# Kernel optimization log

Measured on AMD Instinct MI355X. Metric: run time of the kernel, lower is better.

The kernel has to match this reference:

```python
import jax, jax.numpy as jnp
import numpy as np

B, S, D, H = 8, 2048, 512, 8
DH = D // H


def setup_inputs() -> dict:
    key = jax.random.key(0)
    ks = jax.random.split(key, 7)
    scale = 1.0 / np.sqrt(DH)
    return {
        "sequences": jax.random.normal(ks[0], (B, S, D), dtype=jnp.float32),
        # torch Linear weights: [H, d_head, d_head] (out, in) per head
        "Wq": jax.random.uniform(ks[1], (H, DH, DH), jnp.float32, -scale, scale),
        "bq": jax.random.uniform(ks[2], (H, DH), jnp.float32, -scale, scale),
        "Wk": jax.random.uniform(ks[3], (H, DH, DH), jnp.float32, -scale, scale),
        "bk": jax.random.uniform(ks[4], (H, DH), jnp.float32, -scale, scale),
        "Wv": jax.random.uniform(ks[5], (H, DH, DH), jnp.float32, -scale, scale),
        "bv": jax.random.uniform(ks[6], (H, DH), jnp.float32, -scale, scale),
    }


def reference(sequences, Wq, bq, Wk, bk, Wv, bv):
    # split heads: [B, S, H, DH]
    x = sequences.reshape(B, S, H, DH)
    # per-head Linear: y = x @ W^T + b  (torch convention W is [out, in])
    q = jnp.einsum('bshd,hed->bshe', x, Wq) + bq  # [B,S,H,DH]
    k = jnp.einsum('bshd,hed->bshe', x, Wk) + bk
    v = jnp.einsum('bshd,hed->bshe', x, Wv) + bv
    scores = jnp.einsum('bshe,bthe->bhst', q, k) / jnp.sqrt(jnp.float32(DH))
    attn = jax.nn.softmax(scores, axis=-1)  # [B,H,S,S]
    out = jnp.einsum('bhst,bthd->bshd', attn, v)  # [B,S,H,DH]
    return out.reshape(B, S, D)
```

## Files before the change

### kernel.cpp

```cpp
#include <hip/hip_runtime.h>
#include <hip/hip_bf16.h>
#include <math.h>

#define Bc 8
#define Sc 2048
#define Dc 512
#define Hc 8
#define DHc 64
#define KVB 64
#define NT (Sc / KVB)

#define QSCALE 0.18033688011112042f

typedef __attribute__((ext_vector_type(8))) short short8;
typedef __attribute__((ext_vector_type(4))) float f32x4;
typedef __attribute__((ext_vector_type(16))) float f32x16;
typedef unsigned short u16;
typedef unsigned int u32;

static __device__ __forceinline__ u16 f2bf(float f) {
    union { float f; u32 u; } v; v.f = f;
    u32 r = v.u + 0x7fffu + ((v.u >> 16) & 1u);
    return (u16)(r >> 16);
}

static __device__ __forceinline__ u32 cvtpk(float lo, float hi) {
    u32 r; asm("v_cvt_pk_bf16_f32 %0, %1, %2" : "=v"(r) : "v"(lo), "v"(hi)); return r;
}

static __device__ __forceinline__ void plswap(u32& a, u32& b) {
    asm("v_permlane32_swap_b32 %0, %1" : "+v"(a), "+v"(b));
}

static __device__ __forceinline__ short8 pack8v(const float4& a0, const float4& a1) {
    union { u32 w[4]; short8 s; } u;
    u.w[0] = cvtpk(a0.x, a0.y);
    u.w[1] = cvtpk(a0.z, a0.w);
    u.w[2] = cvtpk(a1.x, a1.y);
    u.w[3] = cvtpk(a1.z, a1.w);
    return u.s;
}

static __device__ __forceinline__ short8 mk8(u32 a, u32 b, u32 c, u32 d) {
    union { u32 w[4]; short8 s; } u;
    u.w[0] = a; u.w[1] = b; u.w[2] = c; u.w[3] = d;
    return u.s;
}

#define GLDS16(g, s) \
    __builtin_amdgcn_global_load_lds((const __attribute__((address_space(1))) void*)(g), \
                                     (__attribute__((address_space(3))) void*)(s), 16, 0, 0)

__global__ __launch_bounds__(256) void prep(
    const float* __restrict__ Wq, const float* __restrict__ bq,
    const float* __restrict__ Wk, const float* __restrict__ bk,
    const float* __restrict__ Wv, const float* __restrict__ bv,
    u16* __restrict__ wb, float* __restrict__ bb)
{
    const int gid = blockIdx.x * 256 + threadIdx.x;
    const float* Ws[3] = {Wq, Wk, Wv};
    const int lane = gid & 63, ds = (gid >> 6) & 1, et = (gid >> 7) & 3;
    const int h = (gid >> 9) & 7, m = gid >> 12;
    const int col = lane & 15, grp = lane >> 4;
    const float* src = Ws[m] + ((size_t)h * DHc + et * 16 + col) * DHc + ds * 32 + grp * 8;
    float4 a0 = ((const float4*)src)[0], a1 = ((const float4*)src)[1];
    const float sc = (m == 0) ? QSCALE : 1.0f;
    union { u32 w[4]; int4 v; } u;
    u.w[0] = cvtpk(a0.x * sc, a0.y * sc);
    u.w[1] = cvtpk(a0.z * sc, a0.w * sc);
    u.w[2] = cvtpk(a1.x * sc, a1.y * sc);
    u.w[3] = cvtpk(a1.z * sc, a1.w * sc);
    *(int4*)(wb + (size_t)gid * 8) = u.v;

    if (gid < 3 * Hc * DHc) {
        const float* bs[3] = {bq, bk, bv};
        const int bm = gid >> 9, rest = gid & 511;
        bb[gid] = bs[bm][rest] * (bm == 0 ? QSCALE : 1.0f);
    }
}

__global__ __launch_bounds__(256) void qkv_proj(
    const float* __restrict__ x, const u16* __restrict__ wb,
    const float* __restrict__ bb,
    u16* __restrict__ qo, u16* __restrict__ ko, u16* __restrict__ vto)
{
    const int tile = blockIdx.x;
    const int h    = blockIdx.y;
    const int tid  = threadIdx.x;
    const int w    = tid >> 6;
    const int lane = tid & 63;
    const int col  = lane & 15;
    const int grp  = lane >> 4;
    const int tok0 = tile * 64;
    const int b    = tok0 >> 11;
    const int sblk = tok0 & 2047;
    const int bh   = b * Hc + h;

    __shared__ u16 vlds[64][72];

    short8 xb[2];
    {
        const float* xr = x + (size_t)(tok0 + w * 16 + col) * Dc + h * DHc;
#pragma unroll
        for (int ds = 0; ds < 2; ++ds) {
            const float4* p = (const float4*)(xr + ds * 32 + grp * 8);
            xb[ds] = pack8v(p[0], p[1]);
        }
    }

#pragma unroll
    for (int m = 0; m < 3; ++m) {
        f32x4 acc[4];
#pragma unroll
        for (int et = 0; et < 4; ++et) acc[et] = (f32x4){0.f, 0.f, 0.f, 0.f};

#pragma unroll
        for (int et = 0; et < 4; ++et)
#pragma unroll
            for (int ds = 0; ds < 2; ++ds) {
                short8 wf = *(const short8*)(wb + ((size_t)((((m * 8 + h) * 4 + et) * 2 + ds) * 64) + lane) * 8);
                acc[et] = __builtin_amdgcn_mfma_f32_16x16x32_bf16(wf, xb[ds], acc[et], 0, 0, 0);
            }

#pragma unroll
        for (int et = 0; et < 4; ++et) {
            float4 bias = *(const float4*)(bb + m * 512 + h * DHc + et * 16 + grp * 4);
            float v0 = acc[et][0] + bias.x, v1 = acc[et][1] + bias.y;
            float v2 = acc[et][2] + bias.z, v3 = acc[et][3] + bias.w;
            if (m < 2) {
                u32 lo = cvtpk(v0, v1), hiw = cvtpk(v2, v3);
                u16* dst = (m == 0 ? qo : ko) +
                           ((size_t)bh * Sc + sblk + w * 16 + col) * DHc + et * 16 + grp * 4;
                int2 pk; pk.x = (int)lo; pk.y = (int)hiw;
                *(int2*)dst = pk;
            } else {
                vlds[et * 16 + grp * 4 + 0][w * 16 + col] = f2bf(v0);
                vlds[et * 16 + grp * 4 + 1][w * 16 + col] = f2bf(v1);
                vlds[et * 16 + grp * 4 + 2][w * 16 + col] = f2bf(v2);
                vlds[et * 16 + grp * 4 + 3][w * 16 + col] = f2bf(v3);
            }
        }
    }
    __syncthreads();

    {
        const int e = tid >> 2, c = tid & 3;
        u16* dv = vto + ((size_t)bh * DHc + e) * Sc + sblk + c * 16;
        *(int4*)dv       = *(const int4*)&vlds[e][c * 16];
        *(int4*)(dv + 8) = *(const int4*)&vlds[e][c * 16 + 8];
    }
}

__global__ __launch_bounds__(256, 4) void attn(
    const u16* __restrict__ q, const u16* __restrict__ k,
    const u16* __restrict__ vt, float* __restrict__ out)
{
    const int flat = blockIdx.y * gridDim.x + blockIdx.x;
    const int cpx  = (gridDim.x * gridDim.y) >> 3;
    const int swz  = (flat & 7) * cpx + (flat >> 3);
    const int qt   = swz & 15;
    const int bh   = swz >> 4;
    const int tid  = threadIdx.x;
    const int wv   = tid >> 6;
    const int l    = tid & 63;
    const int lq   = l & 31;
    const int hi   = l >> 5;
    const int b = bh >> 3, h = bh & 7;

    __shared__ u16 kt[2][KVB * DHc];
    __shared__ u16 vl[2][DHc * KVB];

    const u16* __restrict__ qb = q  + (size_t)bh * Sc * DHc;
    const u16* __restrict__ kb = k  + (size_t)bh * Sc * DHc;
    const u16* __restrict__ vb = vt + (size_t)bh * DHc * Sc;
    const int qrow = qt * 128 + wv * 32 + lq;

    short8 qf[4];
#pragma unroll
    for (int s = 0; s < 4; ++s)
        qf[s] = *(const short8*)(qb + (size_t)qrow * DHc + hi * 8 + 16 * s);

    const int srow = wv * 16 + (l >> 3);
    const int schk = (l & 7) ^ ((l >> 3) & 7);
    const u16* gK = kb + (size_t)srow * DHc + schk * 8;
    const u16* gV = vb + (size_t)srow * Sc  + schk * 8;

#define STAGE(bf, kv0) do {                                          \
        const u16* gk_ = gK + (size_t)(kv0) * DHc;                   \
        const u16* gv_ = gV + (kv0);                                 \
        GLDS16(gk_,            &kt[bf][wv * 1024]);                  \
        GLDS16(gk_ + 8 * DHc,  &kt[bf][wv * 1024 + 512]);            \
        GLDS16(gv_,            &vl[bf][wv * 1024]);                  \
        GLDS16(gv_ + 8 * Sc,   &vl[bf][wv * 1024 + 512]);            \
    } while (0)

    f32x16 o0, o1;
#pragma unroll
    for (int i = 0; i < 16; ++i) { o0[i] = 0.f; o1[i] = 0.f; }
    float ls = 0.f;
    const int swz8 = (lq & 7) * 8;

    STAGE(0, 0);
    asm volatile("s_waitcnt vmcnt(0)" ::: "memory");
    __syncthreads();

    for (int t = 0; t < NT; ++t) {
        if (t + 1 < NT) STAGE((t + 1) & 1, (t + 1) * KVB);
        const u16* Kb = kt[t & 1];
        const u16* Vb = vl[t & 1];

#pragma unroll
        for (int sub = 0; sub < 2; ++sub) {
            const int krow = (sub * 32 + lq) * 64;
            short8 kf0 = *(const short8*)(Kb + krow + (((hi + 0) * 8) ^ swz8));
            short8 kf1 = *(const short8*)(Kb + krow + (((hi + 2) * 8) ^ swz8));
            short8 kf2 = *(const short8*)(Kb + krow + (((hi + 4) * 8) ^ swz8));
            short8 kf3 = *(const short8*)(Kb + krow + (((hi + 6) * 8) ^ swz8));

            f32x16 sA;
#pragma unroll
            for (int i = 0; i < 16; ++i) sA[i] = 0.f;
            __builtin_amdgcn_s_setprio(1);
            sA = __builtin_amdgcn_mfma_f32_32x32x16_bf16(kf0, qf[0], sA, 0, 0, 0);
            sA = __builtin_amdgcn_mfma_f32_32x32x16_bf16(kf1, qf[1], sA, 0, 0, 0);
            sA = __builtin_amdgcn_mfma_f32_32x32x16_bf16(kf2, qf[2], sA, 0, 0, 0);
            sA = __builtin_amdgcn_mfma_f32_32x32x16_bf16(kf3, qf[3], sA, 0, 0, 0);
            __builtin_amdgcn_s_setprio(0);

            float sm[8];
#pragma unroll
            for (int i = 0; i < 16; ++i) sA[i] = __builtin_amdgcn_exp2f(sA[i]);
#pragma unroll
            for (int i = 0; i < 8; ++i) sm[i] = sA[2 * i] + sA[2 * i + 1];
#pragma unroll
            for (int stp = 4; stp > 0; stp >>= 1)
#pragma unroll
                for (int i = 0; i < stp; ++i) sm[i] += sm[i + stp];
            ls += sm[0] + __shfl_xor(sm[0], 32);

            u32 pk0 = cvtpk(sA[0],  sA[1]);
            u32 pk1 = cvtpk(sA[2],  sA[3]);
            u32 pk2 = cvtpk(sA[4],  sA[5]);
            u32 pk3 = cvtpk(sA[6],  sA[7]);
            u32 pk4 = cvtpk(sA[8],  sA[9]);
            u32 pk5 = cvtpk(sA[10], sA[11]);
            u32 pk6 = cvtpk(sA[12], sA[13]);
            u32 pk7 = cvtpk(sA[14], sA[15]);
            plswap(pk0, pk2);  plswap(pk1, pk3);
            plswap(pk4, pk6);  plswap(pk5, pk7);
            short8 pb0 = mk8(pk0, pk1, pk2, pk3);
            short8 pb1 = mk8(pk4, pk5, pk6, pk7);

            const int cb = (sub * 4 + hi) * 8;
            short8 vf00 = *(const short8*)(Vb + lq * 64        + (cb ^ swz8));
            short8 vf01 = *(const short8*)(Vb + lq * 64        + ((cb + 16) ^ swz8));
            short8 vf10 = *(const short8*)(Vb + (32 + lq) * 64 + (cb ^ swz8));
            short8 vf11 = *(const short8*)(Vb + (32 + lq) * 64 + ((cb + 16) ^ swz8));

            __builtin_amdgcn_s_setprio(1);
            o0 = __builtin_amdgcn_mfma_f32_32x32x16_bf16(vf00, pb0, o0, 0, 0, 0);
            o0 = __builtin_amdgcn_mfma_f32_32x32x16_bf16(vf01, pb1, o0, 0, 0, 0);
            o1 = __builtin_amdgcn_mfma_f32_32x32x16_bf16(vf10, pb0, o1, 0, 0, 0);
            o1 = __builtin_amdgcn_mfma_f32_32x32x16_bf16(vf11, pb1, o1, 0, 0, 0);
            __builtin_amdgcn_s_setprio(0);
        }

        asm volatile("s_waitcnt vmcnt(0)" ::: "memory");
        __syncthreads();
    }

    float inv = 1.0f / ls;
    float* ob = out + ((size_t)b * Sc + qrow) * Dc + h * DHc + hi * 4;
#pragma unroll
    for (int g = 0; g < 4; ++g) {
        float4 r0 = { o0[4*g]*inv, o0[4*g+1]*inv, o0[4*g+2]*inv, o0[4*g+3]*inv };
        *(float4*)(ob + 8 * g) = r0;
        float4 r1 = { o1[4*g]*inv, o1[4*g+1]*inv, o1[4*g+2]*inv, o1[4*g+3]*inv };
        *(float4*)(ob + 32 + 8 * g) = r1;
    }
}

extern "C" void kernel_launch(void* const* d_in, const int* in_sizes, int n_in,
                              void* d_out, int out_size, void* d_ws, size_t ws_size,
                              hipStream_t stream)
{
    const float* x  = (const float*)d_in[0];
    const float* Wq = (const float*)d_in[1];
    const float* bq = (const float*)d_in[2];
    const float* Wk = (const float*)d_in[3];
    const float* bk = (const float*)d_in[4];
    const float* Wv = (const float*)d_in[5];
    const float* bv = (const float*)d_in[6];
    float* out = (float*)d_out;

    const size_t elems = (size_t)Bc * Hc * Sc * DHc;
    u16* qbuf  = (u16*)d_ws;
    u16* kbuf  = qbuf + elems;
    u16* vtbuf = kbuf + elems;

    u16*   wb = (u16*)d_out;
    float* bb = (float*)((char*)d_out + 12288 * 8 * sizeof(u16));

    prep<<<48, 256, 0, stream>>>(Wq, bq, Wk, bk, Wv, bv, wb, bb);

    dim3 gp(Bc * Sc / 64, Hc);
    qkv_proj<<<gp, 256, 0, stream>>>(x, wb, bb, qbuf, kbuf, vtbuf);

    dim3 ga(Sc / 128, Bc * Hc);
    attn<<<ga, 256, 0, stream>>>(qbuf, kbuf, vtbuf, out);
}
```

Measured before the change: 190.8 us.

## Prefetch K/V two tiles ahead in attention and double tokens per projection block

The attention loop now issues global-to-LDS loads for tile t+2 right after finishing tile t, and waits with a partial vmcnt so that one stage stays in flight. This replaces the wait-all-then-sync pattern, aiming to hide more load latency behind compute, at the cost of an extra barrier per iteration. Separately, the QKV projection block now handles 128 tokens instead of 64. Each wave loads the weight fragments once and reuses them across two token sets, which halves weight reloads and block count but raises register and LDS usage.

```diff
diff --git a/kernel.cpp b/kernel.cpp
--- a/kernel.cpp
+++ b/kernel.cpp
@@ -79,7 +79,7 @@
     }
 }
 
-__global__ __launch_bounds__(256) void qkv_proj(
+__global__ __launch_bounds__(256, 4) void qkv_proj(
     const float* __restrict__ x, const u16* __restrict__ wb,
     const float* __restrict__ bb,
     u16* __restrict__ qo, u16* __restrict__ ko, u16* __restrict__ vto)
@@ -91,53 +91,70 @@
     const int lane = tid & 63;
     const int col  = lane & 15;
     const int grp  = lane >> 4;
-    const int tok0 = tile * 64;
+    const int tok0 = tile * 128;
     const int b    = tok0 >> 11;
     const int sblk = tok0 & 2047;
     const int bh   = b * Hc + h;
 
-    __shared__ u16 vlds[64][72];
-
-    short8 xb[2];
-    {
-        const float* xr = x + (size_t)(tok0 + w * 16 + col) * Dc + h * DHc;
+    __shared__ u16 vlds[64][136];
+
+    short8 xb[2][2];
+#pragma unroll
+    for (int set = 0; set < 2; ++set) {
+        const float* xr = x + (size_t)(tok0 + w * 32 + set * 16 + col) * Dc + h * DHc;
 #pragma unroll
         for (int ds = 0; ds < 2; ++ds) {
             const float4* p = (const float4*)(xr + ds * 32 + grp * 8);
-            xb[ds] = pack8v(p[0], p[1]);
+            xb[set][ds] = pack8v(p[0], p[1]);
         }
     }
 
 #pragma unroll
     for (int m = 0; m < 3; ++m) {
-        f32x4 acc[4];
-#pragma unroll
-        for (int et = 0; et < 4; ++et) acc[et] = (f32x4){0.f, 0.f, 0.f, 0.f};
-
+        short8 wf[4][2];
 #pragma unroll
         for (int et = 0; et < 4; ++et)
 #pragma unroll
+            for (int ds = 0; ds < 2; ++ds)
+                wf[et][ds] = *(const short8*)(wb +
+                    ((size_t)((((m * 8 + h) * 4 + et) * 2 + ds) * 64) + lane) * 8);
+
+        f32x4 acc[2][4];
+#pragma unroll
+        for (int set = 0; set < 2; ++set)
+#pragma unroll
+            for (int et = 0; et < 4; ++et) acc[set][et] = (f32x4){0.f, 0.f, 0.f, 0.f};
+
+#pragma unroll
+        for (int et = 0; et < 4; ++et)
+#pragma unroll
             for (int ds = 0; ds < 2; ++ds) {
-                short8 wf = *(const short8*)(wb + ((size_t)((((m * 8 + h) * 4 + et) * 2 + ds) * 64) + lane) * 8);
-                acc[et] = __builtin_amdgcn_mfma_f32_16x16x32_bf16(wf, xb[ds], acc[et], 0, 0, 0);
+#pragma unroll
+                for (int set = 0; set < 2; ++set)
+                    acc[set][et] = __builtin_amdgcn_mfma_f32_16x16x32_bf16(
+                        wf[et][ds], xb[set][ds], acc[set][et], 0, 0, 0);
             }
 
 #pragma unroll
         for (int et = 0; et < 4; ++et) {
             float4 bias = *(const float4*)(bb + m * 512 + h * DHc + et * 16 + grp * 4);
-            float v0 = acc[et][0] + bias.x, v1 = acc[et][1] + bias.y;
-            float v2 = acc[et][2] + bias.z, v3 = acc[et][3] + bias.w;
-            if (m < 2) {
-                u32 lo = cvtpk(v0, v1), hiw = cvtpk(v2, v3);
-                u16* dst = (m == 0 ? qo : ko) +
-                           ((size_t)bh * Sc + sblk + w * 16 + col) * DHc + et * 16 + grp * 4;
-                int2 pk; pk.x = (int)lo; pk.y = (int)hiw;
-                *(int2*)dst = pk;
-            } else {
-                vlds[et * 16 + grp * 4 + 0][w * 16 + col] = f2bf(v0);
-                vlds[et * 16 + grp * 4 + 1][w * 16 + col] = f2bf(v1);
-                vlds[et * 16 + grp * 4 + 2][w * 16 + col] = f2bf(v2);
-                vlds[et * 16 + grp * 4 + 3][w * 16 + col] = f2bf(v3);
+#pragma unroll
+            for (int set = 0; set < 2; ++set) {
+                float v0 = acc[set][et][0] + bias.x, v1 = acc[set][et][1] + bias.y;
+                float v2 = acc[set][et][2] + bias.z, v3 = acc[set][et][3] + bias.w;
+                const int trow = w * 32 + set * 16 + col;
+                if (m < 2) {
+                    u32 lo = cvtpk(v0, v1), hiw = cvtpk(v2, v3);
+                    u16* dst = (m == 0 ? qo : ko) +
+                               ((size_t)bh * Sc + sblk + trow) * DHc + et * 16 + grp * 4;
+                    int2 pk; pk.x = (int)lo; pk.y = (int)hiw;
+                    *(int2*)dst = pk;
+                } else {
+                    vlds[et * 16 + grp * 4 + 0][trow] = f2bf(v0);
+                    vlds[et * 16 + grp * 4 + 1][trow] = f2bf(v1);
+                    vlds[et * 16 + grp * 4 + 2][trow] = f2bf(v2);
+                    vlds[et * 16 + grp * 4 + 3][trow] = f2bf(v3);
+                }
             }
         }
     }
@@ -145,9 +162,11 @@
 
     {
         const int e = tid >> 2, c = tid & 3;
-        u16* dv = vto + ((size_t)bh * DHc + e) * Sc + sblk + c * 16;
-        *(int4*)dv       = *(const int4*)&vlds[e][c * 16];
-        *(int4*)(dv + 8) = *(const int4*)&vlds[e][c * 16 + 8];
+        u16* dv = vto + ((size_t)bh * DHc + e) * Sc + sblk + c * 32;
+        const u16* sv = &vlds[e][c * 32];
+#pragma unroll
+        for (int i = 0; i < 4; ++i)
+            *(int4*)(dv + i * 8) = *(const int4*)(sv + i * 8);
     }
 }
 
@@ -201,11 +220,12 @@
     const int swz8 = (lq & 7) * 8;
 
     STAGE(0, 0);
-    asm volatile("s_waitcnt vmcnt(0)" ::: "memory");
-    __syncthreads();
+    STAGE(1, KVB);
+    asm volatile("s_waitcnt vmcnt(4)" ::: "memory");
+    __builtin_amdgcn_s_barrier();
+    __builtin_amdgcn_sched_barrier(0);
 
     for (int t = 0; t < NT; ++t) {
-        if (t + 1 < NT) STAGE((t + 1) & 1, (t + 1) * KVB);
         const u16* Kb = kt[t & 1];
         const u16* Vb = vl[t & 1];
 
@@ -265,8 +285,17 @@
             __builtin_amdgcn_s_setprio(0);
         }
 
-        asm volatile("s_waitcnt vmcnt(0)" ::: "memory");
-        __syncthreads();
+        __builtin_amdgcn_sched_barrier(0);
+        __builtin_amdgcn_s_barrier();
+        __builtin_amdgcn_sched_barrier(0);
+        if (t + 2 < NT) {
+            STAGE(t & 1, (t + 2) * KVB);
+            asm volatile("s_waitcnt vmcnt(4)" ::: "memory");
+        } else {
+            asm volatile("s_waitcnt vmcnt(0)" ::: "memory");
+        }
+        __builtin_amdgcn_s_barrier();
+        __builtin_amdgcn_sched_barrier(0);
     }
 
     float inv = 1.0f / ls;
@@ -303,7 +332,7 @@
 
     prep<<<48, 256, 0, stream>>>(Wq, bq, Wk, bk, Wv, bv, wb, bb);
 
-    dim3 gp(Bc * Sc / 64, Hc);
+    dim3 gp(Bc * Sc / 128, Hc);
     qkv_proj<<<gp, 256, 0, stream>>>(x, wb, bb, qbuf, kbuf, vtbuf);
 
     dim3 ga(Sc / 128, Bc * Hc);
```

Result: no change. 188.2 us (-1.4%).
